# Performance work log

Measured on AMD Instinct MI355X. Metric: run time of the kernel, lower is better.

The kernel has to match this reference:

```python
import jax, jax.numpy as jnp
import numpy as np

INPUT = 28
STEPS = 28
HIDDEN = 128
LABELS = 10
FORGET_BIAS = 1.0


def setup_inputs() -> dict:
    key = jax.random.key(0)
    ks = jax.random.split(key, 4)
    B = 32768
    x = jax.random.normal(ks[0], (B, STEPS, INPUT), dtype=jnp.float32)
    # BasicLSTMCell kernel: [input+hidden, 4*hidden], gate order i, j, f, o
    W_lstm = jax.random.normal(ks[1], (INPUT + HIDDEN, 4 * HIDDEN), dtype=jnp.float32) * 0.08
    b_lstm = jnp.zeros((4 * HIDDEN,), dtype=jnp.float32)
    W_fc = jax.random.normal(ks[2], (HIDDEN, LABELS), dtype=jnp.float32) * 0.08
    b_fc = jnp.zeros((LABELS,), dtype=jnp.float32)
    return {"x": x, "W_lstm": W_lstm, "b_lstm": b_lstm, "W_fc": W_fc, "b_fc": b_fc}


def _lstm_step(carry, x_t, W, b):
    c, h = carry
    gates = jnp.concatenate([x_t, h], axis=-1) @ W + b  # [B, 4H]
    i, j, f, o = jnp.split(gates, 4, axis=-1)
    new_c = c * jax.nn.sigmoid(f + FORGET_BIAS) + jax.nn.sigmoid(i) * jnp.tanh(j)
    new_h = jnp.tanh(new_c) * jax.nn.sigmoid(o)
    return (new_c, new_h), None


def reference(x, W_lstm, b_lstm, W_fc, b_fc):
    B = x.shape[0]
    c0 = jnp.zeros((B, HIDDEN), dtype=x.dtype)
    h0 = jnp.zeros((B, HIDDEN), dtype=x.dtype)
    xs = jnp.swapaxes(x, 0, 1)  # [T, B, INPUT]
    (c, h), _ = jax.lax.scan(lambda carry, xt: _lstm_step(carry, xt, W_lstm, b_lstm), (c0, h0), xs)
    return h @ W_fc + b_fc  # logits [B, LABELS]
```

## Files before the change

kernel.cpp:

```cpp
#include <hip/hip_runtime.h>


typedef _Float16 f16x8 __attribute__((ext_vector_type(8)));
typedef float f32x4 __attribute__((ext_vector_type(4)));

#define HSTRIDE 136
#define L2E 1.44269504f

__global__ __launch_bounds__(512, 2)
void lstm_r18(const float* __restrict__ x,
              const float* __restrict__ W,
              const float* __restrict__ b,
              const float* __restrict__ Wfc,
              const float* __restrict__ bfc,
              float* __restrict__ out)
{
    __shared__ __align__(16) _Float16 h_s[2][128 * HSTRIDE];
    __shared__ __align__(16) _Float16 xs[2][8 * 512];

    const int tid  = threadIdx.x;
    const int wave = tid >> 6;
    const int lane = tid & 63;
    const int m16  = lane & 15;
    const int quad = lane >> 4;
    const int rbase = blockIdx.x * 128;
    const int hc = wave * 16 + m16;
    const bool hipri = (wave & 4) != 0;

    for (int i = tid; i < 128 * HSTRIDE; i += 512) h_s[0][i] = (_Float16)0.0f;
    for (int i = tid; i < 2 * 8 * 512; i += 512) {
        const int q = i & 511;
        const bool bslot = ((q >> 7) == 3) && (((q & 7) == 4) || ((q & 7) == 5));
        ((_Float16*)xs)[i] = bslot ? (_Float16)1.0f : (_Float16)0.0f;
    }

    f16x8 Wx[4];
    f16x8 Wh[4][4];
    #pragma unroll
    for (int g = 0; g < 4; g++) {
        const int col = g * 128 + hc;
        const float sc = (g == 1) ? 2.0f * L2E : -L2E;
        f16x8 w8;
        #pragma unroll
        for (int j = 0; j < 8; j++) {
            const int kk = quad * 8 + j;
            w8[j] = (kk < 28) ? (_Float16)(sc * W[kk * 512 + col]) : (_Float16)0.0f;
        }
        if (quad == 3) {
            const float bv = sc * (b[col] + (g == 2 ? 1.0f : 0.0f));
            const _Float16 hi = (_Float16)bv;
            w8[4] = hi;
            w8[5] = (_Float16)(bv - (float)hi);
        }
        Wx[g] = w8;
        #pragma unroll
        for (int ks = 0; ks < 4; ks++) {
            f16x8 h8;
            #pragma unroll
            for (int j = 0; j < 8; j++)
                h8[j] = (_Float16)(sc * W[(28 + ks * 32 + quad * 8 + j) * 512 + col]);
            Wh[ks][g] = h8;
        }
    }

    __syncthreads();

    const int row16 = (tid >> 3) & 15;
    const int sk    = ((tid >> 7) & 3) * 8 + (tid & 7);
    const bool valid = (sk < 28);
    const int goff0 = (rbase + row16) * 784 + sk;

    #pragma unroll
    for (int e = 0; e < 8; e++)
        if (valid) xs[0][e * 512 + tid] = (_Float16)x[goff0 + e * 12544];
    __syncthreads();

    float creg[32];
    #pragma unroll
    for (int i = 0; i < 32; i++) creg[i] = 0.0f;

    const int foff = quad * 128 + m16 * 8;
    const f32x4 ZERO = (f32x4){0.0f, 0.0f, 0.0f, 0.0f};

    int buf = 0;
    for (int t = 0; t < 28; t++) {
        const int nb = buf ^ 1;

        float xv[8];
        if (t < 27 && valid) {
            const float* xt = x + (t + 1) * 28;
            #pragma unroll
            for (int e = 0; e < 8; e++) xv[e] = xt[goff0 + e * 12544];
        }

        f32x4 acc[2][4];

        {
            if (hipri) __builtin_amdgcn_s_setprio(1);
            f16x8 ax = *(const f16x8*)(&xs[buf][foff]);
            #pragma unroll
            for (int g = 0; g < 4; g++)
                acc[0][g] = __builtin_amdgcn_mfma_f32_16x16x32_f16(ax, Wx[g], ZERO, 0, 0, 0);
            #pragma unroll
            for (int ks = 0; ks < 4; ks++) {
                f16x8 ah = *(const f16x8*)(&h_s[buf][m16 * HSTRIDE + ks * 32 + quad * 8]);
                #pragma unroll
                for (int g = 0; g < 4; g++)
                    acc[0][g] = __builtin_amdgcn_mfma_f32_16x16x32_f16(ah, Wh[ks][g], acc[0][g], 0, 0, 0);
            }
            if (hipri) __builtin_amdgcn_s_setprio(0);
        }

        #pragma unroll
        for (int mt = 0; mt < 8; mt++) {
            const int cur = mt & 1, nxt = cur ^ 1;

            if (mt < 7) {
                if (hipri) __builtin_amdgcn_s_setprio(1);
                f16x8 axn = *(const f16x8*)(&xs[buf][(mt + 1) * 512 + foff]);
                #pragma unroll
                for (int g = 0; g < 4; g++)
                    acc[nxt][g] = __builtin_amdgcn_mfma_f32_16x16x32_f16(axn, Wx[g], ZERO, 0, 0, 0);
                #pragma unroll
                for (int ks = 0; ks < 4; ks++) {
                    f16x8 ahn = *(const f16x8*)(&h_s[buf][((mt + 1) * 16 + m16) * HSTRIDE + ks * 32 + quad * 8]);
                    #pragma unroll
                    for (int g = 0; g < 4; g++)
                        acc[nxt][g] = __builtin_amdgcn_mfma_f32_16x16x32_f16(ahn, Wh[ks][g], acc[nxt][g], 0, 0, 0);
                }
                if (hipri) __builtin_amdgcn_s_setprio(0);
            }

            #pragma unroll
            for (int r = 0; r < 4; r++) {
                float ei  = __builtin_amdgcn_exp2f(acc[cur][0][r]);
                float e2j = __builtin_amdgcn_exp2f(acc[cur][1][r]);
                float ef  = __builtin_amdgcn_exp2f(acc[cur][2][r]);
                float eo  = __builtin_amdgcn_exp2f(acc[cur][3][r]);
                float A   = 1.0f + ei;
                float Bv  = e2j + 1.0f;
                float C   = 1.0f + ef;
                float AB  = A * Bv;
                float rP  = __builtin_amdgcn_rcpf(AB * C);
                float num = __builtin_fmaf(e2j, 2.0f * L2E, -2.0f * L2E);
                float cn  = __builtin_fmaf(creg[mt * 4 + r], AB * rP, num * (C * rP));
                creg[mt * 4 + r] = cn;
                float e2c = __builtin_amdgcn_exp2f(cn);
                float rQ  = __builtin_amdgcn_rcpf((e2c + 1.0f) * (1.0f + eo));
                float hv  = (e2c - 1.0f) * rQ;
                h_s[nb][(mt * 16 + quad * 4 + r) * HSTRIDE + hc] = (_Float16)hv;
            }
        }

        if (t < 27 && valid) {
            #pragma unroll
            for (int e = 0; e < 8; e++)
                xs[nb][e * 512 + tid] = (_Float16)xv[e];
        }
        __syncthreads();
        buf = nb;
    }

    for (int i = tid; i < 1280; i += 512) {
        const int row = i / 10, lab = i % 10;
        float acc = bfc[lab];
        #pragma unroll 8
        for (int k = 0; k < 128; k++)
            acc += (float)h_s[buf][row * HSTRIDE + k] * Wfc[k * 10 + lab];
        out[(size_t)(rbase + row) * 10 + lab] = acc;
    }
}

extern "C" void kernel_launch(void* const* d_in, const int* in_sizes, int n_in,
                              void* d_out, int out_size, void* d_ws, size_t ws_size,
                              hipStream_t stream) {
    const float* x   = (const float*)d_in[0];
    const float* W   = (const float*)d_in[1];
    const float* b   = (const float*)d_in[2];
    const float* Wfc = (const float*)d_in[3];
    const float* bfc = (const float*)d_in[4];
    float* out = (float*)d_out;

    const int B = in_sizes[0] / (28 * 28);
    const int blocks = B / 128;
    lstm_r18<<<blocks, 512, 0, stream>>>(x, W, b, Wfc, bfc, out);
}
```

Baseline: 309.2 us.

## Split waves into MFMA producers and activation consumers with LDS flag handoff

Waves 0-3 now only run the gate matmuls, each covering 32 hidden columns across all row tiles. They write fp32 gate tiles into a double-buffered LDS staging area and raise per-tile flags. Waves 4-7 spin on those flags, read the gates, acknowledge, and compute the cell/hidden activations. The aim is to overlap matrix-core work with transcendental/VALU work through warp specialization. In exchange it adds LDS traffic, spin-wait polling, and doubled weight and cell-state registers per producer or consumer wave, with a risk of register spills or ordering hazards.

Measured after the change: 573.5 us. +85.5%, slower.

```diff
diff --git a/kernel.cpp b/kernel.cpp
--- a/kernel.cpp
+++ b/kernel.cpp
@@ -8,7 +8,7 @@
 #define L2E 1.44269504f
 
 __global__ __launch_bounds__(512, 2)
-void lstm_r18(const float* __restrict__ x,
+void lstm_r21(const float* __restrict__ x,
               const float* __restrict__ W,
               const float* __restrict__ b,
               const float* __restrict__ Wfc,
@@ -17,6 +17,9 @@
 {
     __shared__ __align__(16) _Float16 h_s[2][128 * HSTRIDE];
     __shared__ __align__(16) _Float16 xs[2][8 * 512];
+    __shared__ __align__(16) float gbuf[4][2][8][16][16];
+    __shared__ int flg[4][8];
+    __shared__ int ack[4];
 
     const int tid  = threadIdx.x;
     const int wave = tid >> 6;
@@ -24,8 +27,8 @@
     const int m16  = lane & 15;
     const int quad = lane >> 4;
     const int rbase = blockIdx.x * 128;
-    const int hc = wave * 16 + m16;
-    const bool hipri = (wave & 4) != 0;
+    const bool producer = (wave < 4);
+    const int p = wave & 3;
 
     for (int i = tid; i < 128 * HSTRIDE; i += 512) h_s[0][i] = (_Float16)0.0f;
     for (int i = tid; i < 2 * 8 * 512; i += 512) {
@@ -33,33 +36,37 @@
         const bool bslot = ((q >> 7) == 3) && (((q & 7) == 4) || ((q & 7) == 5));
         ((_Float16*)xs)[i] = bslot ? (_Float16)1.0f : (_Float16)0.0f;
     }
+    if (tid < 32) ((int*)flg)[tid] = 0;
+    if (tid < 4)  ack[tid] = 0;
 
-    f16x8 Wx[4];
-    f16x8 Wh[4][4];
-    #pragma unroll
-    for (int g = 0; g < 4; g++) {
-        const int col = g * 128 + hc;
-        const float sc = (g == 1) ? 2.0f * L2E : -L2E;
-        f16x8 w8;
+    f16x8 Wt[8][5];
+    if (producer) {
         #pragma unroll
-        for (int j = 0; j < 8; j++) {
-            const int kk = quad * 8 + j;
-            w8[j] = (kk < 28) ? (_Float16)(sc * W[kk * 512 + col]) : (_Float16)0.0f;
-        }
-        if (quad == 3) {
-            const float bv = sc * (b[col] + (g == 2 ? 1.0f : 0.0f));
-            const _Float16 hi = (_Float16)bv;
-            w8[4] = hi;
-            w8[5] = (_Float16)(bv - (float)hi);
-        }
-        Wx[g] = w8;
-        #pragma unroll
-        for (int ks = 0; ks < 4; ks++) {
-            f16x8 h8;
+        for (int ct = 0; ct < 8; ct++) {
+            const int g = ct >> 1, half = ct & 1;
+            const int col = g * 128 + p * 32 + half * 16 + m16;
+            const float sc = (g == 1) ? 2.0f * L2E : -L2E;
+            f16x8 w8;
             #pragma unroll
-            for (int j = 0; j < 8; j++)
-                h8[j] = (_Float16)(sc * W[(28 + ks * 32 + quad * 8 + j) * 512 + col]);
-            Wh[ks][g] = h8;
+            for (int j = 0; j < 8; j++) {
+                const int kk = quad * 8 + j;
+                w8[j] = (kk < 28) ? (_Float16)(sc * W[kk * 512 + col]) : (_Float16)0.0f;
+            }
+            if (quad == 3) {
+                const float bv = sc * (b[col] + (g == 2 ? 1.0f : 0.0f));
+                const _Float16 hi = (_Float16)bv;
+                w8[4] = hi;
+                w8[5] = (_Float16)(bv - (float)hi);
+            }
+            Wt[ct][0] = w8;
+            #pragma unroll
+            for (int ks = 0; ks < 4; ks++) {
+                f16x8 h8;
+                #pragma unroll
+                for (int j = 0; j < 8; j++)
+                    h8[j] = (_Float16)(sc * W[(28 + ks * 32 + quad * 8 + j) * 512 + col]);
+                Wt[ct][ks + 1] = h8;
+            }
         }
     }
 
@@ -75,12 +82,12 @@
         if (valid) xs[0][e * 512 + tid] = (_Float16)x[goff0 + e * 12544];
     __syncthreads();
 
-    float creg[32];
-    #pragma unroll
-    for (int i = 0; i < 32; i++) creg[i] = 0.0f;
-
     const int foff = quad * 128 + m16 * 8;
     const f32x4 ZERO = (f32x4){0.0f, 0.0f, 0.0f, 0.0f};
+
+    float creg[64];
+    #pragma unroll
+    for (int i = 0; i < 64; i++) creg[i] = 0.0f;
 
     int buf = 0;
     for (int t = 0; t < 28; t++) {
@@ -93,62 +100,64 @@
             for (int e = 0; e < 8; e++) xv[e] = xt[goff0 + e * 12544];
         }
 
-        f32x4 acc[2][4];
-
-        {
-            if (hipri) __builtin_amdgcn_s_setprio(1);
-            f16x8 ax = *(const f16x8*)(&xs[buf][foff]);
-            #pragma unroll
-            for (int g = 0; g < 4; g++)
-                acc[0][g] = __builtin_amdgcn_mfma_f32_16x16x32_f16(ax, Wx[g], ZERO, 0, 0, 0);
-            #pragma unroll
-            for (int ks = 0; ks < 4; ks++) {
-                f16x8 ah = *(const f16x8*)(&h_s[buf][m16 * HSTRIDE + ks * 32 + quad * 8]);
+        if (producer) {
+            for (int rt = 0; rt < 8; rt++) {
+                if (rt >= 2) {
+                    const int need = t * 8 + rt - 1;
+                    while (*(volatile int*)&ack[p] < need)
+                        __builtin_amdgcn_s_sleep(1);
+                }
+                f16x8 ax = *(const f16x8*)(&xs[buf][rt * 512 + foff]);
+                f16x8 ah0 = *(const f16x8*)(&h_s[buf][(rt * 16 + m16) * HSTRIDE + 0 * 32 + quad * 8]);
+                f16x8 ah1 = *(const f16x8*)(&h_s[buf][(rt * 16 + m16) * HSTRIDE + 1 * 32 + quad * 8]);
+                f16x8 ah2 = *(const f16x8*)(&h_s[buf][(rt * 16 + m16) * HSTRIDE + 2 * 32 + quad * 8]);
+                f16x8 ah3 = *(const f16x8*)(&h_s[buf][(rt * 16 + m16) * HSTRIDE + 3 * 32 + quad * 8]);
+                #pragma unroll
+                for (int ct = 0; ct < 8; ct++) {
+                    f32x4 acc = __builtin_amdgcn_mfma_f32_16x16x32_f16(ax,  Wt[ct][0], ZERO, 0, 0, 0);
+                    acc = __builtin_amdgcn_mfma_f32_16x16x32_f16(ah0, Wt[ct][1], acc, 0, 0, 0);
+                    acc = __builtin_amdgcn_mfma_f32_16x16x32_f16(ah1, Wt[ct][2], acc, 0, 0, 0);
+                    acc = __builtin_amdgcn_mfma_f32_16x16x32_f16(ah2, Wt[ct][3], acc, 0, 0, 0);
+                    acc = __builtin_amdgcn_mfma_f32_16x16x32_f16(ah3, Wt[ct][4], acc, 0, 0, 0);
+                    *(f32x4*)&gbuf[p][rt & 1][ct][m16][quad * 4] = acc;
+                }
+                asm volatile("s_waitcnt lgkmcnt(0)" ::: "memory");
+                if (lane == 0) *(volatile int*)&flg[p][rt] = t + 1;
+            }
+        } else {
+            for (int rt = 0; rt < 8; rt++) {
+                while (*(volatile int*)&flg[p][rt] < t + 1) { }
+                f32x4 gv[4][2];
                 #pragma unroll
                 for (int g = 0; g < 4; g++)
-                    acc[0][g] = __builtin_amdgcn_mfma_f32_16x16x32_f16(ah, Wh[ks][g], acc[0][g], 0, 0, 0);
-            }
-            if (hipri) __builtin_amdgcn_s_setprio(0);
-        }
+                    #pragma unroll
+                    for (int half = 0; half < 2; half++)
+                        gv[g][half] = *(const f32x4*)&gbuf[p][rt & 1][g * 2 + half][m16][quad * 4];
+                asm volatile("s_waitcnt lgkmcnt(0)" ::: "memory");
+                if (lane == 0) *(volatile int*)&ack[p] = t * 8 + rt + 1;
 
-        #pragma unroll
-        for (int mt = 0; mt < 8; mt++) {
-            const int cur = mt & 1, nxt = cur ^ 1;
-
-            if (mt < 7) {
-                if (hipri) __builtin_amdgcn_s_setprio(1);
-                f16x8 axn = *(const f16x8*)(&xs[buf][(mt + 1) * 512 + foff]);
                 #pragma unroll
-                for (int g = 0; g < 4; g++)
-                    acc[nxt][g] = __builtin_amdgcn_mfma_f32_16x16x32_f16(axn, Wx[g], ZERO, 0, 0, 0);
-                #pragma unroll
-                for (int ks = 0; ks < 4; ks++) {
-                    f16x8 ahn = *(const f16x8*)(&h_s[buf][((mt + 1) * 16 + m16) * HSTRIDE + ks * 32 + quad * 8]);
+                for (int half = 0; half < 2; half++)
                     #pragma unroll
-                    for (int g = 0; g < 4; g++)
-                        acc[nxt][g] = __builtin_amdgcn_mfma_f32_16x16x32_f16(ahn, Wh[ks][g], acc[nxt][g], 0, 0, 0);
-                }
-                if (hipri) __builtin_amdgcn_s_setprio(0);
-            }
-
-            #pragma unroll
-            for (int r = 0; r < 4; r++) {
-                float ei  = __builtin_amdgcn_exp2f(acc[cur][0][r]);
-                float e2j = __builtin_amdgcn_exp2f(acc[cur][1][r]);
-                float ef  = __builtin_amdgcn_exp2f(acc[cur][2][r]);
-                float eo  = __builtin_amdgcn_exp2f(acc[cur][3][r]);
-                float A   = 1.0f + ei;
-                float Bv  = e2j + 1.0f;
-                float C   = 1.0f + ef;
-                float AB  = A * Bv;
-                float rP  = __builtin_amdgcn_rcpf(AB * C);
-                float num = __builtin_fmaf(e2j, 2.0f * L2E, -2.0f * L2E);
-                float cn  = __builtin_fmaf(creg[mt * 4 + r], AB * rP, num * (C * rP));
-                creg[mt * 4 + r] = cn;
-                float e2c = __builtin_amdgcn_exp2f(cn);
-                float rQ  = __builtin_amdgcn_rcpf((e2c + 1.0f) * (1.0f + eo));
-                float hv  = (e2c - 1.0f) * rQ;
-                h_s[nb][(mt * 16 + quad * 4 + r) * HSTRIDE + hc] = (_Float16)hv;
+                    for (int r = 0; r < 4; r++) {
+                        float ei  = __builtin_amdgcn_exp2f(gv[0][half][r]);
+                        float e2j = __builtin_amdgcn_exp2f(gv[1][half][r]);
+                        float ef  = __builtin_amdgcn_exp2f(gv[2][half][r]);
+                        float eo  = __builtin_amdgcn_exp2f(gv[3][half][r]);
+                        float A   = 1.0f + ei;
+                        float Bv  = e2j + 1.0f;
+                        float C   = 1.0f + ef;
+                        float AB  = A * Bv;
+                        float rP  = __builtin_amdgcn_rcpf(AB * C);
+                        float num = __builtin_fmaf(e2j, 2.0f * L2E, -2.0f * L2E);
+                        const int ci = rt * 8 + half * 4 + r;
+                        float cn  = __builtin_fmaf(creg[ci], AB * rP, num * (C * rP));
+                        creg[ci] = cn;
+                        float e2c = __builtin_amdgcn_exp2f(cn);
+                        float rQ  = __builtin_amdgcn_rcpf((e2c + 1.0f) * (1.0f + eo));
+                        float hv  = (e2c - 1.0f) * rQ;
+                        h_s[nb][(rt * 16 + quad * 4 + r) * HSTRIDE + p * 32 + half * 16 + m16] = (_Float16)hv;
+                    }
             }
         }
 
@@ -183,5 +192,5 @@
 
     const int B = in_sizes[0] / (28 * 28);
     const int blocks = B / 128;
-    lstm_r18<<<blocks, 512, 0, stream>>>(x, W, b, Wfc, bfc, out);
+    lstm_r21<<<blocks, 512, 0, stream>>>(x, W, b, Wfc, bfc, out);
 }
```
